# Kernel tuning notes

Measured on AMD Instinct MI355X. Metric: run time of the kernel, lower is better.

Reference implementation:

```python
import jax, jax.numpy as jnp
import numpy as np

B, C, T = 4, 1024, 2048
H = 16            # num_heads
G = 32            # GroupNorm groups (normalization(channels) == GroupNorm(32, C))
EPS = 1e-5


def setup_inputs() -> dict:
    key = jax.random.key(0)
    ks = jax.random.split(key, 7)
    x = jax.random.normal(ks[0], (B, C, T), dtype=jnp.float32)
    gn_scale = jax.random.normal(ks[1], (C,), dtype=jnp.float32) * 0.02 + 1.0
    gn_bias = jax.random.normal(ks[2], (C,), dtype=jnp.float32) * 0.02
    qkv_w = jax.random.normal(ks[3], (3 * C, C), dtype=jnp.float32) / np.sqrt(C)
    qkv_b = jax.random.normal(ks[4], (3 * C,), dtype=jnp.float32) * 0.02
    # NOTE: original zero-inits proj_out; randomized here so output != x for testing.
    proj_w = jax.random.normal(ks[5], (C, C), dtype=jnp.float32) / np.sqrt(C)
    proj_b = jax.random.normal(ks[6], (C,), dtype=jnp.float32) * 0.02
    return {"x": x, "gn_scale": gn_scale, "gn_bias": gn_bias,
            "qkv_w": qkv_w, "qkv_b": qkv_b, "proj_w": proj_w, "proj_b": proj_b}


def reference(x, gn_scale, gn_bias, qkv_w, qkv_b, proj_w, proj_b):
    b, c, t = x.shape
    ch = c // H
    # GroupNorm(32, C) over (channels-in-group, T)
    xg = x.reshape(b, G, c // G, t)
    mean = xg.mean(axis=(2, 3), keepdims=True)
    var = xg.var(axis=(2, 3), keepdims=True)
    xn = ((xg - mean) * jax.lax.rsqrt(var + EPS)).reshape(b, c, t)
    xn = xn * gn_scale[None, :, None] + gn_bias[None, :, None]
    # 1x1 conv QKV: [B, 3C, T]
    qkv = jnp.einsum('oc,bct->bot', qkv_w, xn) + qkv_b[None, :, None]
    q, k, v = jnp.split(qkv, 3, axis=1)
    # split heads -> [B*H, ch, T]
    q = q.reshape(b * H, ch, t)
    k = k.reshape(b * H, ch, t)
    v = v.reshape(b * H, ch, t)
    scale = 1.0 / np.sqrt(np.sqrt(ch)).astype(np.float32)
    # full T x T attention weights, softmax in fp32 (as original)
    w = jnp.einsum('bct,bcs->bts', q * scale, k * scale)
    w = jax.nn.softmax(w.astype(jnp.float32), axis=-1).astype(w.dtype)
    a = jnp.einsum('bts,bcs->bct', w, v).reshape(b, c, t)
    # 1x1 conv projection + residual
    h = jnp.einsum('oc,bct->bot', proj_w, a) + proj_b[None, :, None]
    return x + h
```

## Files before the change

kernel.cpp:

```cpp
#include <hip/hip_runtime.h>
#include <hip/hip_bf16.h>
#include <stdint.h>

#define Bn 4
#define Cn 1024
#define Tn 2048
#define Hn 16
#define Gn 32
#define SCALE_Q 0.18033688f

typedef short short8  __attribute__((ext_vector_type(8)));
typedef short short4_t __attribute__((ext_vector_type(4)));
typedef float float4_t __attribute__((ext_vector_type(4)));

__device__ __forceinline__ short f2bf(float f) {
    uint32_t u = __float_as_uint(f);
    uint32_t r = (u + 0x7FFFu + ((u >> 16) & 1u)) >> 16;
    return (short)r;
}

__device__ __forceinline__ float exp2_fast(float x) {
#if __has_builtin(__builtin_amdgcn_exp2f)
    return __builtin_amdgcn_exp2f(x);
#else
    return exp2f(x);
#endif
}

__device__ __forceinline__ uint32_t pack_bf16_trunc(float lo, float hi) {
#if __has_builtin(__builtin_amdgcn_perm)
    return __builtin_amdgcn_perm(__float_as_uint(hi), __float_as_uint(lo), 0x07060302u);
#else
    return (__float_as_uint(lo) >> 16) | (__float_as_uint(hi) & 0xFFFF0000u);
#endif
}

#define GLL16(gptr, lptr)                                                      \
    __builtin_amdgcn_global_load_lds(                                          \
        (const __attribute__((address_space(1))) unsigned int*)(gptr),         \
        (__attribute__((address_space(3))) unsigned int*)(lptr), 16, 0, 0)

__global__ __launch_bounds__(256) void cvt_w(const float* __restrict__ src,
                                             short* __restrict__ dst, int n4) {
    int i = blockIdx.x * 256 + threadIdx.x;
    if (i < n4) {
        float4_t v = reinterpret_cast<const float4_t*>(src)[i];
        short4_t o;
        o[0] = f2bf(v[0]); o[1] = f2bf(v[1]); o[2] = f2bf(v[2]); o[3] = f2bf(v[3]);
        reinterpret_cast<short4_t*>(dst)[i] = o;
    }
}

__global__ __launch_bounds__(256) void groupnorm_k(const float* __restrict__ x,
                                                   const float* __restrict__ gs,
                                                   const float* __restrict__ gb,
                                                   short* __restrict__ xnT) {
    int blk = blockIdx.x;
    int b = blk >> 5, g = blk & 31;
    const float* base = x + ((size_t)(b * Cn + g * 32)) * Tn;
    int tid = threadIdx.x;

    float s = 0.f, ss = 0.f;
    const float4_t* b4 = reinterpret_cast<const float4_t*>(base);
    for (int i = tid; i < 16384; i += 256) {
        float4_t v = b4[i];
        s  += v[0] + v[1] + v[2] + v[3];
        ss += v[0]*v[0] + v[1]*v[1] + v[2]*v[2] + v[3]*v[3];
    }
    #pragma unroll
    for (int m = 1; m < 64; m <<= 1) { s += __shfl_xor(s, m); ss += __shfl_xor(ss, m); }
    __shared__ float red[8];
    int wave = tid >> 6;
    if ((tid & 63) == 0) { red[wave * 2] = s; red[wave * 2 + 1] = ss; }
    __syncthreads();
    float ts  = red[0] + red[2] + red[4] + red[6];
    float tss = red[1] + red[3] + red[5] + red[7];
    float mean = ts * (1.f / 65536.f);
    float var  = tss * (1.f / 65536.f) - mean * mean;
    float rstd = rsqrtf(var + 1e-5f);

    __shared__ float tile[64][33];
    for (int t0 = 0; t0 < Tn; t0 += 64) {
        #pragma unroll
        for (int k = 0; k < 8; k++) {
            int e = tid + k * 256;
            int c = e >> 6, tt = e & 63;
            float v = base[c * Tn + t0 + tt];
            tile[tt][c] = (v - mean) * rstd * gs[g * 32 + c] + gb[g * 32 + c];
        }
        __syncthreads();
        #pragma unroll
        for (int k = 0; k < 8; k++) {
            int f = tid + k * 256;
            int tt = f >> 5, c = f & 31;
            xnT[((size_t)(b * Tn + t0 + tt)) * Cn + g * 32 + c] = f2bf(tile[tt][c]);
        }
        __syncthreads();
    }
}

template <int MODE>
__global__ __launch_bounds__(256) void gemm_k(const short* __restrict__ W,
                                              const short* __restrict__ Bm,
                                              const float* __restrict__ bias,
                                              const float* __restrict__ xres,
                                              short* __restrict__ qkT,
                                              short* __restrict__ vbuf,
                                              float* __restrict__ outp) {
    constexpr int K = 1024;
    __shared__ short As[128 * 64];
    __shared__ short Bs[128 * 64];
    int m0 = blockIdx.x * 128, n0 = blockIdx.y * 128, b = blockIdx.z;
    int tid = threadIdx.x;
    int wave = tid >> 6, lane = tid & 63, quad = lane >> 4, l15 = lane & 15;
    int wm = wave >> 1, wn = wave & 1;
    const short* Ab = W + (size_t)m0 * K;
    const short* Bb = Bm + ((size_t)b * Tn + n0) * K;

    float4_t acc[4][4];
    float4_t z = {0.f, 0.f, 0.f, 0.f};
    #pragma unroll
    for (int i = 0; i < 4; i++)
        #pragma unroll
        for (int j = 0; j < 4; j++) acc[i][j] = z;

    int sw = l15 & 7;

    for (int k0 = 0; k0 < K; k0 += 64) {
        #pragma unroll
        for (int r = 0; r < 4; r++) {
            int cid = r * 256 + tid;
            int row = cid >> 3, j = cid & 7;
            int chunk = j ^ (row & 7);
            GLL16(Ab + (size_t)row * K + k0 + chunk * 8, As + cid * 8);
            GLL16(Bb + (size_t)row * K + k0 + chunk * 8, Bs + cid * 8);
        }
        __syncthreads();
        #pragma unroll
        for (int kk = 0; kk < 2; kk++) {
            short8 af[4], bfg[4];
            #pragma unroll
            for (int mi = 0; mi < 4; mi++)
                af[mi] = *reinterpret_cast<const short8*>(
                    &As[(wm * 64 + mi * 16 + l15) * 64 + ((4 * kk + quad) ^ sw) * 8]);
            #pragma unroll
            for (int ni = 0; ni < 4; ni++)
                bfg[ni] = *reinterpret_cast<const short8*>(
                    &Bs[(wn * 64 + ni * 16 + l15) * 64 + ((4 * kk + quad) ^ sw) * 8]);
            #pragma unroll
            for (int mi = 0; mi < 4; mi++)
                #pragma unroll
                for (int ni = 0; ni < 4; ni++)
                    acc[mi][ni] = __builtin_amdgcn_mfma_f32_16x16x32_bf16(
                        af[mi], bfg[ni], acc[mi][ni], 0, 0, 0);
        }
        __syncthreads();
    }

    if (MODE == 0) {
        #pragma unroll
        for (int mi = 0; mi < 4; mi++) {
            int mrow = m0 + wm * 64 + mi * 16 + quad * 4;
            #pragma unroll
            for (int ni = 0; ni < 4; ni++) {
                int t = n0 + wn * 64 + ni * 16 + l15;
                if (mrow < 2048) {
                    int hh = mrow >> 6, ch = mrow & 63;
                    float sc = (mrow < 1024) ? SCALE_Q : 1.0f;
                    short4_t pk;
                    #pragma unroll
                    for (int r = 0; r < 4; r++)
                        pk[r] = f2bf((acc[mi][ni][r] + bias[mrow + r]) * sc);
                    *reinterpret_cast<short4_t*>(
                        &qkT[(((size_t)b * 32 + hh) * Tn + t) * 64 + ch]) = pk;
                } else {
                    int c = mrow - 2048;
                    #pragma unroll
                    for (int r = 0; r < 4; r++)
                        vbuf[((size_t)b * Cn + c + r) * Tn + t] =
                            f2bf(acc[mi][ni][r] + bias[mrow + r]);
                }
            }
        }
    } else {
        #pragma unroll
        for (int mi = 0; mi < 4; mi++) {
            int mrow = m0 + wm * 64 + mi * 16 + quad * 4;
            #pragma unroll
            for (int ni = 0; ni < 4; ni++) {
                int t = n0 + wn * 64 + ni * 16 + l15;
                #pragma unroll
                for (int r = 0; r < 4; r++) {
                    size_t idx = ((size_t)b * Cn + mrow + r) * Tn + t;
                    outp[idx] = xres[idx] + bias[mrow + r] + acc[mi][ni][r];
                }
            }
        }
    }
}

__global__ __launch_bounds__(256, 2) void attn_k(const short* __restrict__ qkT,
                                                 const short* __restrict__ vbuf,
                                                 short* __restrict__ aT) {
    __shared__ short ks[64 * 72];
    __shared__ short vs[64 * 72];
    __shared__ short ps[4][64 * 72];
    int bh = blockIdx.y; int b = bh >> 4, h = bh & 15;
    int t0 = blockIdx.x * 256;
    int tid = threadIdx.x;
    int wave = tid >> 6, lane = tid & 63, quad = lane >> 4, l15 = lane & 15;
    const short* qb = qkT + (((size_t)b * 32 + h) * Tn) * 64;
    const short* kb = qkT + (((size_t)b * 32 + 16 + h) * Tn) * 64;
    const short* vb = vbuf + ((size_t)b * Cn + h * 64) * Tn;
    int tw = t0 + wave * 64;
    short* psw = &ps[wave][0];

    short8 qf[4][2];
    #pragma unroll
    for (int tni = 0; tni < 4; tni++)
        #pragma unroll
        for (int kk = 0; kk < 2; kk++)
            qf[tni][kk] = *reinterpret_cast<const short8*>(
                qb + ((size_t)(tw + tni * 16 + l15)) * 64 + kk * 32 + quad * 8);

    short8 ones;
    #pragma unroll
    for (int i = 0; i < 8; i++) ones[i] = (short)0x3F80;

    float4_t z = {0.f, 0.f, 0.f, 0.f};
    float4_t acc[4][4], accl[4];
    #pragma unroll
    for (int i = 0; i < 4; i++) {
        accl[i] = z;
        #pragma unroll
        for (int j = 0; j < 4; j++) acc[i][j] = z;
    }

    for (int s0 = 0; s0 < Tn; s0 += 64) {
        #pragma unroll
        for (int r = 0; r < 2; r++) {
            int cid = r * 256 + tid;
            int row = cid >> 3, off = cid & 7;
            *reinterpret_cast<uint4*>(&ks[row * 72 + off * 8]) =
                *reinterpret_cast<const uint4*>(kb + ((size_t)(s0 + row)) * 64 + off * 8);
            *reinterpret_cast<uint4*>(&vs[row * 72 + off * 8]) =
                *reinterpret_cast<const uint4*>(vb + (size_t)row * Tn + s0 + off * 8);
        }
        __syncthreads();

        #pragma unroll
        for (int smi = 0; smi < 4; smi++) {
            float4_t sa[4];
            #pragma unroll
            for (int tni = 0; tni < 4; tni++) sa[tni] = z;
            #pragma unroll
            for (int kk = 0; kk < 2; kk++) {
                short8 kf = *reinterpret_cast<const short8*>(
                    &ks[(smi * 16 + l15) * 72 + kk * 32 + quad * 8]);
                #pragma unroll
                for (int tni = 0; tni < 4; tni++)
                    sa[tni] = __builtin_amdgcn_mfma_f32_16x16x32_bf16(
                        kf, qf[tni][kk], sa[tni], 0, 0, 0);
            }
            #pragma unroll
            for (int tni = 0; tni < 4; tni++) {
                float p0 = exp2_fast(sa[tni][0]);
                float p1 = exp2_fast(sa[tni][1]);
                float p2 = exp2_fast(sa[tni][2]);
                float p3 = exp2_fast(sa[tni][3]);
                uint2 pk;
                pk.x = pack_bf16_trunc(p0, p1);
                pk.y = pack_bf16_trunc(p2, p3);
                *reinterpret_cast<uint2*>(
                    &psw[(tni * 16 + l15) * 72 + smi * 16 + quad * 4]) = pk;
            }
        }
        asm volatile("s_waitcnt lgkmcnt(0)" ::: "memory");

        #pragma unroll
        for (int kk = 0; kk < 2; kk++) {
            short8 vf[4];
            #pragma unroll
            for (int ci = 0; ci < 4; ci++)
                vf[ci] = *reinterpret_cast<const short8*>(
                    &vs[(ci * 16 + l15) * 72 + kk * 32 + quad * 8]);
            #pragma unroll
            for (int tmi = 0; tmi < 4; tmi++) {
                short8 pf = *reinterpret_cast<const short8*>(
                    &psw[(tmi * 16 + l15) * 72 + kk * 32 + quad * 8]);
                accl[tmi] = __builtin_amdgcn_mfma_f32_16x16x32_bf16(
                    pf, ones, accl[tmi], 0, 0, 0);
                #pragma unroll
                for (int ci = 0; ci < 4; ci++)
                    acc[tmi][ci] = __builtin_amdgcn_mfma_f32_16x16x32_bf16(
                        pf, vf[ci], acc[tmi][ci], 0, 0, 0);
            }
        }
        __syncthreads();
    }

    #pragma unroll
    for (int tmi = 0; tmi < 4; tmi++) {
        float rl[4];
        #pragma unroll
        for (int r = 0; r < 4; r++) rl[r] = 1.0f / accl[tmi][r];
        #pragma unroll
        for (int ci = 0; ci < 4; ci++)
            #pragma unroll
            for (int r = 0; r < 4; r++) {
                int t = tw + tmi * 16 + quad * 4 + r;
                int ch = ci * 16 + l15;
                aT[((size_t)b * Tn + t) * Cn + h * 64 + ch] =
                    f2bf(acc[tmi][ci][r] * rl[r]);
            }
    }
}

extern "C" void kernel_launch(void* const* d_in, const int* in_sizes, int n_in,
                              void* d_out, int out_size, void* d_ws, size_t ws_size,
                              hipStream_t stream) {
    const float* x     = (const float*)d_in[0];
    const float* gs    = (const float*)d_in[1];
    const float* gb    = (const float*)d_in[2];
    const float* qkvw  = (const float*)d_in[3];
    const float* qkvb  = (const float*)d_in[4];
    const float* projw = (const float*)d_in[5];
    const float* projb = (const float*)d_in[6];
    float* out = (float*)d_out;

    char* ws = (char*)d_ws;
    short* wqkv  = (short*)(ws + 0);
    short* wproj = (short*)(ws + 6291456);
    short* xnT   = (short*)(ws + 8388608);
    short* aT    = (short*)(ws + 8388608);
    short* qkT   = (short*)(ws + 25165824);
    short* vbuf  = (short*)(ws + 58720256);

    cvt_w<<<dim3(3072), dim3(256), 0, stream>>>(qkvw, wqkv, 786432);
    cvt_w<<<dim3(1024), dim3(256), 0, stream>>>(projw, wproj, 262144);
    groupnorm_k<<<dim3(Bn * Gn), dim3(256), 0, stream>>>(x, gs, gb, xnT);
    gemm_k<0><<<dim3(24, 16, 4), dim3(256), 0, stream>>>(wqkv, xnT, qkvb, nullptr,
                                                         qkT, vbuf, nullptr);
    attn_k<<<dim3(8, 64), dim3(256), 0, stream>>>(qkT, vbuf, aT);
    gemm_k<1><<<dim3(8, 16, 4), dim3(256), 0, stream>>>(wproj, aT, projb, x,
                                                        nullptr, nullptr, out);
}
```

Before: 338.6 us.

## Read K/V fragments directly from global memory in attention, drop shared staging and barriers

The attention kernel stops staging K and V tiles in shared memory and loads MFMA fragments straight from global memory (relying on L1/L2 caching). This removes both __syncthreads per KV tile and shrinks the per-wave P buffer by processing 32-key halves, so occupancy is raised to 3 blocks per SM. The trade-off is that each wave now fetches K/V independently, with no shared reuse across the 4 waves, and global loads have higher latency, which can stall the MFMA chain.

```diff
diff --git a/kernel.cpp b/kernel.cpp
--- a/kernel.cpp
+++ b/kernel.cpp
@@ -199,12 +199,10 @@
     }
 }
 
-__global__ __launch_bounds__(256, 2) void attn_k(const short* __restrict__ qkT,
+__global__ __launch_bounds__(256, 3) void attn_k(const short* __restrict__ qkT,
                                                  const short* __restrict__ vbuf,
                                                  short* __restrict__ aT) {
-    __shared__ short ks[64 * 72];
-    __shared__ short vs[64 * 72];
-    __shared__ short ps[4][64 * 72];
+    __shared__ short ps[4][2][64 * 40];
     int bh = blockIdx.y; int b = bh >> 4, h = bh & 15;
     int t0 = blockIdx.x * 256;
     int tid = threadIdx.x;
@@ -213,7 +211,6 @@
     const short* kb = qkT + (((size_t)b * 32 + 16 + h) * Tn) * 64;
     const short* vb = vbuf + ((size_t)b * Cn + h * 64) * Tn;
     int tw = t0 + wave * 64;
-    short* psw = &ps[wave][0];
 
     short8 qf[4][2];
     #pragma unroll
@@ -238,56 +235,48 @@
 
     for (int s0 = 0; s0 < Tn; s0 += 64) {
         #pragma unroll
-        for (int r = 0; r < 2; r++) {
-            int cid = r * 256 + tid;
-            int row = cid >> 3, off = cid & 7;
-            *reinterpret_cast<uint4*>(&ks[row * 72 + off * 8]) =
-                *reinterpret_cast<const uint4*>(kb + ((size_t)(s0 + row)) * 64 + off * 8);
-            *reinterpret_cast<uint4*>(&vs[row * 72 + off * 8]) =
-                *reinterpret_cast<const uint4*>(vb + (size_t)row * Tn + s0 + off * 8);
-        }
-        __syncthreads();
-
-        #pragma unroll
-        for (int smi = 0; smi < 4; smi++) {
-            float4_t sa[4];
-            #pragma unroll
-            for (int tni = 0; tni < 4; tni++) sa[tni] = z;
-            #pragma unroll
-            for (int kk = 0; kk < 2; kk++) {
-                short8 kf = *reinterpret_cast<const short8*>(
-                    &ks[(smi * 16 + l15) * 72 + kk * 32 + quad * 8]);
-                #pragma unroll
-                for (int tni = 0; tni < 4; tni++)
-                    sa[tni] = __builtin_amdgcn_mfma_f32_16x16x32_bf16(
-                        kf, qf[tni][kk], sa[tni], 0, 0, 0);
-            }
-            #pragma unroll
-            for (int tni = 0; tni < 4; tni++) {
-                float p0 = exp2_fast(sa[tni][0]);
-                float p1 = exp2_fast(sa[tni][1]);
-                float p2 = exp2_fast(sa[tni][2]);
-                float p3 = exp2_fast(sa[tni][3]);
-                uint2 pk;
-                pk.x = pack_bf16_trunc(p0, p1);
-                pk.y = pack_bf16_trunc(p2, p3);
-                *reinterpret_cast<uint2*>(
-                    &psw[(tni * 16 + l15) * 72 + smi * 16 + quad * 4]) = pk;
-            }
-        }
-        asm volatile("s_waitcnt lgkmcnt(0)" ::: "memory");
-
-        #pragma unroll
-        for (int kk = 0; kk < 2; kk++) {
+        for (int half = 0; half < 2; half++) {
+            short* psw = &ps[wave][half][0];
+            int sbase = s0 + half * 32;
+
+            #pragma unroll
+            for (int sm = 0; sm < 2; sm++) {
+                float4_t sa[4];
+                #pragma unroll
+                for (int tni = 0; tni < 4; tni++) sa[tni] = z;
+                #pragma unroll
+                for (int kk = 0; kk < 2; kk++) {
+                    short8 kf = *reinterpret_cast<const short8*>(
+                        kb + ((size_t)(sbase + sm * 16 + l15)) * 64 + kk * 32 + quad * 8);
+                    #pragma unroll
+                    for (int tni = 0; tni < 4; tni++)
+                        sa[tni] = __builtin_amdgcn_mfma_f32_16x16x32_bf16(
+                            kf, qf[tni][kk], sa[tni], 0, 0, 0);
+                }
+                #pragma unroll
+                for (int tni = 0; tni < 4; tni++) {
+                    float p0 = exp2_fast(sa[tni][0]);
+                    float p1 = exp2_fast(sa[tni][1]);
+                    float p2 = exp2_fast(sa[tni][2]);
+                    float p3 = exp2_fast(sa[tni][3]);
+                    uint2 pk;
+                    pk.x = pack_bf16_trunc(p0, p1);
+                    pk.y = pack_bf16_trunc(p2, p3);
+                    *reinterpret_cast<uint2*>(
+                        &psw[(tni * 16 + l15) * 40 + sm * 16 + quad * 4]) = pk;
+                }
+            }
+            asm volatile("s_waitcnt lgkmcnt(0)" ::: "memory");
+
             short8 vf[4];
             #pragma unroll
             for (int ci = 0; ci < 4; ci++)
                 vf[ci] = *reinterpret_cast<const short8*>(
-                    &vs[(ci * 16 + l15) * 72 + kk * 32 + quad * 8]);
+                    vb + (size_t)(ci * 16 + l15) * Tn + sbase + quad * 8);
             #pragma unroll
             for (int tmi = 0; tmi < 4; tmi++) {
                 short8 pf = *reinterpret_cast<const short8*>(
-                    &psw[(tmi * 16 + l15) * 72 + kk * 32 + quad * 8]);
+                    &psw[(tmi * 16 + l15) * 40 + quad * 8]);
                 accl[tmi] = __builtin_amdgcn_mfma_f32_16x16x32_bf16(
                     pf, ones, accl[tmi], 0, 0, 0);
                 #pragma unroll
@@ -296,7 +285,6 @@
                         pf, vf[ci], acc[tmi][ci], 0, 0, 0);
             }
         }
-        __syncthreads();
     }
 
     #pragma unroll
```

Measured after the change: 383.2 us. 13.2% more time.
